# Optimization experiments

Measured on AMD Instinct MI355X. Metric: run time of the kernel, lower is better.

Reference implementation:

```python
import jax, jax.numpy as jnp
import numpy as np

N = 500000     # total nodes across all sets
DIM = 128      # input feature dim
HID = 128      # hidden_dim (output of key_net/val_net)
KDIM = 128     # key_storage.encoder.input_dim
MID = 128      # build_mlp mid width (midmult=1.0 -> (in+out)/2)
NB = 4096      # n_batches

def mish(x):
    return x * jnp.tanh(jax.nn.softplus(x))

def layernorm(x, g, b):
    mu = jnp.mean(x, axis=-1, keepdims=True)
    var = jnp.var(x, axis=-1, keepdims=True)
    return (x - mu) * jax.lax.rsqrt(var + 1e-5) * g + b

def mlp2(x, W1, b1, g, bn, W2, b2):
    # build_mlp(nlayers=2, layernorm=True, nonlinearity=Mish)
    h = layernorm(x @ W1 + b1, g, bn)
    return mish(h) @ W2 + b2

def seg_softmax(x, batch, n):
    # scatter_softmax over the node axis within each segment, per feature
    m = jax.ops.segment_max(x, batch, num_segments=n)
    e = jnp.exp(x - m[batch])
    d = jax.ops.segment_sum(e, batch, num_segments=n)
    return e / d[batch]

def _init(key, fan_in, shape):
    return jax.random.normal(key, shape, dtype=jnp.float32) / np.sqrt(fan_in)

def setup_inputs():
    key = jax.random.key(0)
    ks = jax.random.split(key, 12)
    return {
        "x": jax.random.normal(ks[0], (N, DIM), dtype=jnp.float32),
        "batch": jnp.sort(jax.random.randint(ks[1], (N,), 0, NB)),
        "n_batches": NB,
        # mapping: Linear(dim -> KDIM)
        "W_map": _init(ks[2], DIM, (DIM, KDIM)), "b_map": jnp.zeros(KDIM, jnp.float32),
        # key_net: KDIM -> MID -> HID
        "kW1": _init(ks[3], KDIM, (KDIM, MID)), "kb1": jnp.zeros(MID, jnp.float32),
        "kg": jnp.ones(MID, jnp.float32), "kbn": jnp.zeros(MID, jnp.float32),
        "kW2": _init(ks[4], MID, (MID, HID)), "kb2": jnp.zeros(HID, jnp.float32),
        # val_net: DIM -> MID -> HID
        "vW1": _init(ks[5], DIM, (DIM, MID)), "vb1": jnp.zeros(MID, jnp.float32),
        "vg": jnp.ones(MID, jnp.float32), "vbn": jnp.zeros(MID, jnp.float32),
        "vW2": _init(ks[6], MID, (MID, HID)), "vb2": jnp.zeros(HID, jnp.float32),
        # inner key_storage encoder params (same structure, on keys)
        "iW_map": _init(ks[7], KDIM, (KDIM, KDIM)), "ib_map": jnp.zeros(KDIM, jnp.float32),
        "ikW1": _init(ks[8], KDIM, (KDIM, MID)), "ikb1": jnp.zeros(MID, jnp.float32),
        "ikg": jnp.ones(MID, jnp.float32), "ikbn": jnp.zeros(MID, jnp.float32),
        "ikW2": _init(ks[9], MID, (MID, HID)), "ikb2": jnp.zeros(HID, jnp.float32),
        "ivW1": _init(ks[10], KDIM, (KDIM, MID)), "ivb1": jnp.zeros(MID, jnp.float32),
        "ivg": jnp.ones(MID, jnp.float32), "ivbn": jnp.zeros(MID, jnp.float32),
        "ivW2": _init(ks[11], MID, (MID, HID)), "ivb2": jnp.zeros(HID, jnp.float32),
    }

def reference(x, batch, n_batches, W_map, b_map, kW1, kb1, kg, kbn, kW2, kb2,
              vW1, vb1, vg, vbn, vW2, vb2, iW_map, ib_map,
              ikW1, ikb1, ikg, ikbn, ikW2, ikb2, ivW1, ivb1, ivg, ivbn, ivW2, ivb2):
    # key0 = mapping(x); keys = scatter_softmax(key0, batch)
    key0 = x @ W_map + b_map                      # [N, KDIM]
    keys = seg_softmax(key0, batch, n_batches)    # [N, KDIM]
    # y = val_net(x) * key_net(keys); z = scatter_sum(y, batch)
    y = mlp2(x, vW1, vb1, vg, vbn, vW2, vb2) * mlp2(keys, kW1, kb1, kg, kbn, kW2, kb2)
    z = jax.ops.segment_sum(y, batch, num_segments=n_batches)   # [NB, HID]
    # keyenc = key_storage.encoder(keys, batch): same encoder math applied to keys
    key0b = keys @ iW_map + ib_map
    keys2 = seg_softmax(key0b, batch, n_batches)
    y2 = mlp2(keys, ivW1, ivb1, ivg, ivbn, ivW2, ivb2) * mlp2(keys2, ikW1, ikb1, ikg, ikbn, ikW2, ikb2)
    keyenc = jax.ops.segment_sum(y2, batch, num_segments=n_batches)  # [NB, HID]
    return (z, keyenc)
```

## Files before the change

### kernel.cpp

```cpp
#include <hip/hip_runtime.h>

typedef _Float16 f16;
typedef _Float16 f16x4 __attribute__((ext_vector_type(4)));
typedef _Float16 f16x8 __attribute__((ext_vector_type(8)));
typedef float f32x4 __attribute__((ext_vector_type(4)));

#define NBATCH 4096
#define RMAX 200

__device__ __forceinline__ f32x4 mfma16(f16x8 a, f16x8 b, f32x4 c) {
  return __builtin_amdgcn_mfma_f32_16x16x32_f16(a, b, c, 0, 0, 0);
}

__device__ __forceinline__ int swz(int r, int c) { return r * 128 + (c ^ ((r & 7) << 3)); }

__global__ void seg_bounds(const int* __restrict__ batch, int N, int NB, int* __restrict__ seg) {
  int s = blockIdx.x * blockDim.x + threadIdx.x;
  if (s > NB) return;
  int lo = 0, hi = N;
  while (lo < hi) { int mid = (lo + hi) >> 1; if (batch[mid] < s) lo = mid + 1; else hi = mid; }
  seg[s] = lo;
}

__global__ void pack_weights(const float* w0, const float* w1, const float* w2, const float* w3,
                             const float* w4, const float* w5, const float* w6, const float* w7,
                             const float* w8, const float* w9, f16* __restrict__ Wp) {
  int idx = blockIdx.x * blockDim.x + threadIdx.x;
  if (idx >= 10 * 16384) return;
  int w = idx >> 14, p = idx & 16383;
  int j = p & 7, lane = (p >> 3) & 63, nt = (p >> 9) & 7, kk = p >> 12;
  int k = kk * 32 + (lane >> 4) * 8 + j;
  int n = nt * 16 + (lane & 15);
  const float* W;
  switch (w) {
    case 0: W = w0; break; case 1: W = w1; break; case 2: W = w2; break;
    case 3: W = w3; break; case 4: W = w4; break; case 5: W = w5; break;
    case 6: W = w6; break; case 7: W = w7; break; case 8: W = w8; break;
    default: W = w9; break;
  }
  Wp[idx] = (f16)W[k * 128 + n];
}

__device__ __forceinline__ void gemm_bias_phase(const f16* S, f16* D, const f16* __restrict__ Wg,
    const float* __restrict__ bias, int rows, int mh, int nq, int lane, int quad, int li) {
  int ntl = (rows + 15) >> 4;
  f16x8 bF[4][2];
#pragma unroll
  for (int kk = 0; kk < 4; ++kk)
#pragma unroll
    for (int j = 0; j < 2; ++j)
      bF[kk][j] = *(const f16x8*)(Wg + (size_t)(((kk * 8 + nq * 2 + j) * 64 + lane) * 8));
  float bc[2];
#pragma unroll
  for (int j = 0; j < 2; ++j) bc[j] = bias[(nq * 2 + j) * 16 + li];
  for (int t = mh; t < ntl; t += 2) {
    int m0 = t * 16;
    f32x4 acc0 = {0.f, 0.f, 0.f, 0.f}, acc1 = {0.f, 0.f, 0.f, 0.f};
    int rl = m0 + li;
    bool ok = rl < rows;
#pragma unroll
    for (int kk = 0; kk < 4; ++kk) {
      f16x8 aF = {};
      if (ok) aF = *(const f16x8*)(S + swz(rl, kk * 32 + quad * 8));
      acc0 = mfma16(aF, bF[kk][0], acc0);
      acc1 = mfma16(aF, bF[kk][1], acc1);
    }
#pragma unroll
    for (int r = 0; r < 4; ++r) {
      int row = m0 + quad * 4 + r;
      if (row < rows) {
        D[swz(row, (nq * 2) * 16 + li)] = (f16)(acc0[r] + bc[0]);
        D[swz(row, (nq * 2 + 1) * 16 + li)] = (f16)(acc1[r] + bc[1]);
      }
    }
  }
}

__device__ __forceinline__ void ln_mish_pass(f16* D, const float* __restrict__ g,
                                             const float* __restrict__ bn, int rows, int tid) {
  int part = tid & 3;
  float gv[32], bv[32];
#pragma unroll
  for (int j = 0; j < 8; ++j) {
    float4 gg = *(const float4*)(g + part * 32 + j * 4);
    float4 bb = *(const float4*)(bn + part * 32 + j * 4);
    gv[j * 4 + 0] = gg.x; gv[j * 4 + 1] = gg.y; gv[j * 4 + 2] = gg.z; gv[j * 4 + 3] = gg.w;
    bv[j * 4 + 0] = bb.x; bv[j * 4 + 1] = bb.y; bv[j * 4 + 2] = bb.z; bv[j * 4 + 3] = bb.w;
  }
  for (int r = tid >> 2; r < rows; r += 128) {
    f16x8 v[4];
    float s1 = 0.f, s2 = 0.f;
#pragma unroll
    for (int j = 0; j < 4; ++j) {
      v[j] = *(const f16x8*)(D + swz(r, part * 32 + j * 8));
#pragma unroll
      for (int e = 0; e < 8; ++e) { float f = (float)v[j][e]; s1 += f; s2 += f * f; }
    }
    s1 += __shfl_xor(s1, 1, 64); s2 += __shfl_xor(s2, 1, 64);
    s1 += __shfl_xor(s1, 2, 64); s2 += __shfl_xor(s2, 2, 64);
    float mean = s1 * (1.f / 128.f);
    float var = s2 * (1.f / 128.f) - mean * mean;
    float rstd = rsqrtf(var + 1e-5f);
#pragma unroll
    for (int j = 0; j < 4; ++j) {
      f16x8 o;
#pragma unroll
      for (int e = 0; e < 8; ++e) {
        float u = ((float)v[j][e] - mean) * rstd * gv[j * 8 + e] + bv[j * 8 + e];
        float t = __expf(u);
        float w = t * t + 2.f * t;
        float res = (u > 20.f) ? u : u * (w / (w + 2.f));
        o[e] = (f16)res;
      }
      *(f16x8*)(D + swz(r, part * 32 + j * 8)) = o;
    }
  }
}

__device__ __forceinline__ void softmax_phase(f16* P, int rows, int tid, float* sm, float* sd) {
  int c = tid & 127, st = tid >> 7;
  float m = -3.4e38f, d = 0.f;
#pragma unroll 4
  for (int r = st; r < rows; r += 4) {
    float v = (float)P[swz(r, c)];
    if (v > m) { d = d * __expf(m - v) + 1.f; m = v; } else d += __expf(v - m);
  }
  sm[st * 128 + c] = m; sd[st * 128 + c] = d;
  __syncthreads();
  if (tid < 128) {
    float M = sm[tid], D = sd[tid];
#pragma unroll
    for (int k = 1; k < 4; ++k) {
      float mk = sm[k * 128 + tid], dk = sd[k * 128 + tid];
      if (mk > M) { D = D * __expf(M - mk) + dk; M = mk; } else D += dk * __expf(mk - M);
    }
    sm[tid] = M; sd[tid] = (D > 0.f) ? 1.f / D : 0.f;
  }
  __syncthreads();
  float M = sm[c], inv = sd[c];
#pragma unroll 4
  for (int r = st; r < rows; r += 4)
    P[swz(r, c)] = (f16)(__expf((float)P[swz(r, c)] - M) * inv);
  __syncthreads();
}

__device__ __forceinline__ void pairsum_phase(const f16* S1, const f16* __restrict__ W1,
    const float* __restrict__ b1, const f16* S2, const f16* __restrict__ W2,
    const float* __restrict__ b2, float* __restrict__ outp, int s, int rows,
    int mh, int nq, int lane, int quad, int li, float* red, int tid) {
  f16x8 bF1[4][2], bF2[4][2];
#pragma unroll
  for (int kk = 0; kk < 4; ++kk)
#pragma unroll
    for (int j = 0; j < 2; ++j) {
      size_t off = (size_t)(((kk * 8 + nq * 2 + j) * 64 + lane) * 8);
      bF1[kk][j] = *(const f16x8*)(W1 + off);
      bF2[kk][j] = *(const f16x8*)(W2 + off);
    }
  float b1c[2], b2c[2];
#pragma unroll
  for (int j = 0; j < 2; ++j) {
    b1c[j] = b1[(nq * 2 + j) * 16 + li];
    b2c[j] = b2[(nq * 2 + j) * 16 + li];
  }
  float zs0 = 0.f, zs1 = 0.f;
  int ntl = (rows + 15) >> 4;
  for (int t = mh; t < ntl; t += 2) {
    int m0 = t * 16;
    f32x4 a10 = {0.f,0.f,0.f,0.f}, a11 = {0.f,0.f,0.f,0.f};
    f32x4 a20 = {0.f,0.f,0.f,0.f}, a21 = {0.f,0.f,0.f,0.f};
    int rl = m0 + li;
    bool ok = rl < rows;
#pragma unroll
    for (int kk = 0; kk < 4; ++kk) {
      f16x8 aF1 = {}, aF2 = {};
      if (ok) {
        aF1 = *(const f16x8*)(S1 + swz(rl, kk * 32 + quad * 8));
        aF2 = *(const f16x8*)(S2 + swz(rl, kk * 32 + quad * 8));
      }
      a10 = mfma16(aF1, bF1[kk][0], a10);
      a11 = mfma16(aF1, bF1[kk][1], a11);
      a20 = mfma16(aF2, bF2[kk][0], a20);
      a21 = mfma16(aF2, bF2[kk][1], a21);
    }
    float cs0 = 0.f, cs1 = 0.f;
#pragma unroll
    for (int r = 0; r < 4; ++r) {
      int row = m0 + quad * 4 + r;
      if (row < rows) {
        cs0 += (a10[r] + b1c[0]) * (a20[r] + b2c[0]);
        cs1 += (a11[r] + b1c[1]) * (a21[r] + b2c[1]);
      }
    }
    cs0 += __shfl_xor(cs0, 16, 64); cs0 += __shfl_xor(cs0, 32, 64);
    cs1 += __shfl_xor(cs1, 16, 64); cs1 += __shfl_xor(cs1, 32, 64);
    zs0 += cs0; zs1 += cs1;
  }
  red[tid] = 0.f; red[tid + 512] = 0.f;
  __syncthreads();
  if (quad == 0) {
    int w = tid >> 6;
    red[w * 128 + (nq * 2) * 16 + li] = zs0;
    red[w * 128 + (nq * 2 + 1) * 16 + li] = zs1;
  }
  __syncthreads();
  if (tid < 128) {
    float ssum = 0.f;
#pragma unroll
    for (int w = 0; w < 8; ++w) ssum += red[w * 128 + tid];
    outp[(size_t)s * 128 + tid] = ssum;
  }
  __syncthreads();
}

__global__ __launch_bounds__(512) void encoder_mega(
    const float* __restrict__ x, const int* __restrict__ seg, const f16* __restrict__ Wp,
    const float* b_map, const float* kb1, const float* kg, const float* kbn, const float* kb2,
    const float* vb1, const float* vg, const float* vbn, const float* vb2,
    const float* ib_map, const float* ikb1, const float* ikg, const float* ikbn,
    const float* ikb2, const float* ivb1, const float* ivg, const float* ivbn,
    const float* ivb2, float* __restrict__ Z, float* __restrict__ KE) {
  __shared__ f16 L0[RMAX * 128];
  __shared__ f16 L1[RMAX * 128];
  __shared__ f16 L2[RMAX * 128];
  __shared__ float red[8 * 128];
  __shared__ float sm[512];
  __shared__ float sd[512];
  int s = blockIdx.x;
  int a = seg[s], e = seg[s + 1];
  int rows = e - a;
  int tid = threadIdx.x;
  if (rows <= 0) {
    if (tid < 128) {
      Z[(size_t)s * 128 + tid] = 0.f;
      KE[(size_t)s * 128 + tid] = 0.f;
    }
    return;
  }
  if (rows > RMAX) rows = RMAX;
  int lane = tid & 63, wave = tid >> 6, quad = lane >> 4, li = lane & 15;
  int mh = wave & 1, nq = wave >> 1;

  const float* xa = x + (size_t)a * 128;
  for (int i = tid * 4; i < rows * 128; i += 2048) {
    float4 v = *(const float4*)(xa + i);
    f16x4 h;
    h[0] = (f16)v.x; h[1] = (f16)v.y; h[2] = (f16)v.z; h[3] = (f16)v.w;
    *(f16x4*)(L0 + swz(i >> 7, i & 127)) = h;
  }
  __syncthreads();
  gemm_bias_phase(L0, L1, Wp + 0 * 16384, b_map, rows, mh, nq, lane, quad, li);
  __syncthreads();
  softmax_phase(L1, rows, tid, sm, sd);
  gemm_bias_phase(L0, L2, Wp + 3 * 16384, vb1, rows, mh, nq, lane, quad, li);
  __syncthreads();
  ln_mish_pass(L2, vg, vbn, rows, tid);
  __syncthreads();
  gemm_bias_phase(L1, L0, Wp + 1 * 16384, kb1, rows, mh, nq, lane, quad, li);
  __syncthreads();
  ln_mish_pass(L0, kg, kbn, rows, tid);
  __syncthreads();
  pairsum_phase(L2, Wp + 4 * 16384, vb2, L0, Wp + 2 * 16384, kb2, Z, s, rows,
                mh, nq, lane, quad, li, red, tid);
  gemm_bias_phase(L1, L2, Wp + 5 * 16384, ib_map, rows, mh, nq, lane, quad, li);
  __syncthreads();
  softmax_phase(L2, rows, tid, sm, sd);
  gemm_bias_phase(L1, L0, Wp + 8 * 16384, ivb1, rows, mh, nq, lane, quad, li);
  __syncthreads();
  ln_mish_pass(L0, ivg, ivbn, rows, tid);
  __syncthreads();
  gemm_bias_phase(L2, L1, Wp + 6 * 16384, ikb1, rows, mh, nq, lane, quad, li);
  __syncthreads();
  ln_mish_pass(L1, ikg, ikbn, rows, tid);
  __syncthreads();
  pairsum_phase(L0, Wp + 9 * 16384, ivb2, L1, Wp + 7 * 16384, ikb2, KE, s, rows,
                mh, nq, lane, quad, li, red, tid);
}

extern "C" void kernel_launch(void* const* d_in, const int* in_sizes, int n_in,
                              void* d_out, int out_size, void* d_ws, size_t ws_size,
                              hipStream_t stream) {
  const float* x = (const float*)d_in[0];
  const int* batch = (const int*)d_in[1];
  const int N = in_sizes[1];
  const float* W_map = (const float*)d_in[3];  const float* b_map = (const float*)d_in[4];
  const float* kW1 = (const float*)d_in[5];    const float* kb1 = (const float*)d_in[6];
  const float* kg = (const float*)d_in[7];     const float* kbn = (const float*)d_in[8];
  const float* kW2 = (const float*)d_in[9];    const float* kb2 = (const float*)d_in[10];
  const float* vW1 = (const float*)d_in[11];   const float* vb1 = (const float*)d_in[12];
  const float* vg = (const float*)d_in[13];    const float* vbn = (const float*)d_in[14];
  const float* vW2 = (const float*)d_in[15];   const float* vb2 = (const float*)d_in[16];
  const float* iW_map = (const float*)d_in[17];const float* ib_map = (const float*)d_in[18];
  const float* ikW1 = (const float*)d_in[19];  const float* ikb1 = (const float*)d_in[20];
  const float* ikg = (const float*)d_in[21];   const float* ikbn = (const float*)d_in[22];
  const float* ikW2 = (const float*)d_in[23];  const float* ikb2 = (const float*)d_in[24];
  const float* ivW1 = (const float*)d_in[25];  const float* ivb1 = (const float*)d_in[26];
  const float* ivg = (const float*)d_in[27];   const float* ivbn = (const float*)d_in[28];
  const float* ivW2 = (const float*)d_in[29];  const float* ivb2 = (const float*)d_in[30];

  char* ws = (char*)d_ws;
  int* seg = (int*)ws;
  f16* Wp = (f16*)(ws + 32768);

  float* Z = (float*)d_out;
  float* KE = Z + (out_size / 2);

  seg_bounds<<<(NBATCH + 1 + 255) / 256, 256, 0, stream>>>(batch, N, NBATCH, seg);
  pack_weights<<<(10 * 16384) / 256, 256, 0, stream>>>(
      W_map, kW1, kW2, vW1, vW2, iW_map, ikW1, ikW2, ivW1, ivW2, Wp);

  encoder_mega<<<NBATCH, 512, 0, stream>>>(
      x, seg, Wp, b_map, kb1, kg, kbn, kb2, vb1, vg, vbn, vb2,
      ib_map, ikb1, ikg, ikbn, ikb2, ivb1, ivg, ivbn, ivb2, Z, KE);
}
```

Before: 1.287 ms.

## Double block size to 1024 threads and restructure segment softmax into register two-pass

Launches the fused encoder with 1024 threads per segment. Each wave now covers one of four row-tile phases, so every GEMM phase gets twice as many waves in flight. LayerNorm-Mish becomes single-row-per-thread, since 256 row slots cover RMAX, and weight-parameter loads move inside the row guard. Softmax now holds up to 25 values per thread in registers and computes max, then sum, then normalise, replacing the online max/sum. This avoids rereading LDS and the conditional exp rescaling, at the cost of more registers and extra barriers. Per-block register budget halves and the reduction scratch grows, which may reduce occupancy.

```diff
diff --git a/kernel.cpp b/kernel.cpp
--- a/kernel.cpp
+++ b/kernel.cpp
@@ -42,7 +42,7 @@
 }
 
 __device__ __forceinline__ void gemm_bias_phase(const f16* S, f16* D, const f16* __restrict__ Wg,
-    const float* __restrict__ bias, int rows, int mh, int nq, int lane, int quad, int li) {
+    const float* __restrict__ bias, int rows, int mq, int nq, int lane, int quad, int li) {
   int ntl = (rows + 15) >> 4;
   f16x8 bF[4][2];
 #pragma unroll
@@ -53,7 +53,7 @@
   float bc[2];
 #pragma unroll
   for (int j = 0; j < 2; ++j) bc[j] = bias[(nq * 2 + j) * 16 + li];
-  for (int t = mh; t < ntl; t += 2) {
+  for (int t = mq; t < ntl; t += 4) {
     int m0 = t * 16;
     f32x4 acc0 = {0.f, 0.f, 0.f, 0.f}, acc1 = {0.f, 0.f, 0.f, 0.f};
     int rl = m0 + li;
@@ -79,15 +79,16 @@
 __device__ __forceinline__ void ln_mish_pass(f16* D, const float* __restrict__ g,
                                              const float* __restrict__ bn, int rows, int tid) {
   int part = tid & 3;
-  float gv[32], bv[32];
-#pragma unroll
-  for (int j = 0; j < 8; ++j) {
-    float4 gg = *(const float4*)(g + part * 32 + j * 4);
-    float4 bb = *(const float4*)(bn + part * 32 + j * 4);
-    gv[j * 4 + 0] = gg.x; gv[j * 4 + 1] = gg.y; gv[j * 4 + 2] = gg.z; gv[j * 4 + 3] = gg.w;
-    bv[j * 4 + 0] = bb.x; bv[j * 4 + 1] = bb.y; bv[j * 4 + 2] = bb.z; bv[j * 4 + 3] = bb.w;
-  }
-  for (int r = tid >> 2; r < rows; r += 128) {
+  int r = tid >> 2;
+  if (r < rows) {
+    float gv[32], bv[32];
+#pragma unroll
+    for (int j = 0; j < 8; ++j) {
+      float4 gg = *(const float4*)(g + part * 32 + j * 4);
+      float4 bb = *(const float4*)(bn + part * 32 + j * 4);
+      gv[j * 4 + 0] = gg.x; gv[j * 4 + 1] = gg.y; gv[j * 4 + 2] = gg.z; gv[j * 4 + 3] = gg.w;
+      bv[j * 4 + 0] = bb.x; bv[j * 4 + 1] = bb.y; bv[j * 4 + 2] = bb.z; bv[j * 4 + 3] = bb.w;
+    }
     f16x8 v[4];
     float s1 = 0.f, s2 = 0.f;
 #pragma unroll
@@ -117,37 +118,53 @@
   }
 }
 
-__device__ __forceinline__ void softmax_phase(f16* P, int rows, int tid, float* sm, float* sd) {
+__device__ __forceinline__ void softmax_phase(f16* P, int rows, int tid, float* scr) {
   int c = tid & 127, st = tid >> 7;
-  float m = -3.4e38f, d = 0.f;
-#pragma unroll 4
-  for (int r = st; r < rows; r += 4) {
-    float v = (float)P[swz(r, c)];
-    if (v > m) { d = d * __expf(m - v) + 1.f; m = v; } else d += __expf(v - m);
-  }
-  sm[st * 128 + c] = m; sd[st * 128 + c] = d;
+  float v[25];
+#pragma unroll
+  for (int i = 0; i < 25; ++i) {
+    int r = st + i * 8;
+    v[i] = (r < rows) ? (float)P[swz(r, c)] : -3.4e38f;
+  }
+  float m = v[0];
+#pragma unroll
+  for (int i = 1; i < 25; ++i) m = fmaxf(m, v[i]);
+  scr[st * 128 + c] = m;
   __syncthreads();
   if (tid < 128) {
-    float M = sm[tid], D = sd[tid];
-#pragma unroll
-    for (int k = 1; k < 4; ++k) {
-      float mk = sm[k * 128 + tid], dk = sd[k * 128 + tid];
-      if (mk > M) { D = D * __expf(M - mk) + dk; M = mk; } else D += dk * __expf(mk - M);
-    }
-    sm[tid] = M; sd[tid] = (D > 0.f) ? 1.f / D : 0.f;
-  }
-  __syncthreads();
-  float M = sm[c], inv = sd[c];
-#pragma unroll 4
-  for (int r = st; r < rows; r += 4)
-    P[swz(r, c)] = (f16)(__expf((float)P[swz(r, c)] - M) * inv);
+    float M = scr[tid];
+#pragma unroll
+    for (int k = 1; k < 8; ++k) M = fmaxf(M, scr[k * 128 + tid]);
+    scr[tid] = M;
+  }
+  __syncthreads();
+  float M = scr[c];
+  float d = 0.f;
+#pragma unroll
+  for (int i = 0; i < 25; ++i) { v[i] = __expf(v[i] - M); d += v[i]; }
+  __syncthreads();
+  scr[st * 128 + c] = d;
+  __syncthreads();
+  if (tid < 128) {
+    float D = 0.f;
+#pragma unroll
+    for (int k = 0; k < 8; ++k) D += scr[k * 128 + tid];
+    scr[tid] = (D > 0.f) ? 1.f / D : 0.f;
+  }
+  __syncthreads();
+  float inv = scr[c];
+#pragma unroll
+  for (int i = 0; i < 25; ++i) {
+    int r = st + i * 8;
+    if (r < rows) P[swz(r, c)] = (f16)(v[i] * inv);
+  }
   __syncthreads();
 }
 
 __device__ __forceinline__ void pairsum_phase(const f16* S1, const f16* __restrict__ W1,
     const float* __restrict__ b1, const f16* S2, const f16* __restrict__ W2,
     const float* __restrict__ b2, float* __restrict__ outp, int s, int rows,
-    int mh, int nq, int lane, int quad, int li, float* red, int tid) {
+    int mq, int nq, int lane, int quad, int li, float* red, int tid) {
   f16x8 bF1[4][2], bF2[4][2];
 #pragma unroll
   for (int kk = 0; kk < 4; ++kk)
@@ -165,7 +182,7 @@
   }
   float zs0 = 0.f, zs1 = 0.f;
   int ntl = (rows + 15) >> 4;
-  for (int t = mh; t < ntl; t += 2) {
+  for (int t = mq; t < ntl; t += 4) {
     int m0 = t * 16;
     f32x4 a10 = {0.f,0.f,0.f,0.f}, a11 = {0.f,0.f,0.f,0.f};
     f32x4 a20 = {0.f,0.f,0.f,0.f}, a21 = {0.f,0.f,0.f,0.f};
@@ -196,24 +213,24 @@
     cs1 += __shfl_xor(cs1, 16, 64); cs1 += __shfl_xor(cs1, 32, 64);
     zs0 += cs0; zs1 += cs1;
   }
-  red[tid] = 0.f; red[tid + 512] = 0.f;
+  int wave = tid >> 6;
+  red[tid] = 0.f; red[tid + 1024] = 0.f;
   __syncthreads();
   if (quad == 0) {
-    int w = tid >> 6;
-    red[w * 128 + (nq * 2) * 16 + li] = zs0;
-    red[w * 128 + (nq * 2 + 1) * 16 + li] = zs1;
+    red[wave * 128 + (nq * 2) * 16 + li] = zs0;
+    red[wave * 128 + (nq * 2 + 1) * 16 + li] = zs1;
   }
   __syncthreads();
   if (tid < 128) {
     float ssum = 0.f;
 #pragma unroll
-    for (int w = 0; w < 8; ++w) ssum += red[w * 128 + tid];
+    for (int w = 0; w < 16; ++w) ssum += red[w * 128 + tid];
     outp[(size_t)s * 128 + tid] = ssum;
   }
   __syncthreads();
 }
 
-__global__ __launch_bounds__(512) void encoder_mega(
+__global__ __launch_bounds__(1024) void encoder_mega(
     const float* __restrict__ x, const int* __restrict__ seg, const f16* __restrict__ Wp,
     const float* b_map, const float* kb1, const float* kg, const float* kbn, const float* kb2,
     const float* vb1, const float* vg, const float* vbn, const float* vb2,
@@ -223,9 +240,7 @@
   __shared__ f16 L0[RMAX * 128];
   __shared__ f16 L1[RMAX * 128];
   __shared__ f16 L2[RMAX * 128];
-  __shared__ float red[8 * 128];
-  __shared__ float sm[512];
-  __shared__ float sd[512];
+  __shared__ float scr[2048];
   int s = blockIdx.x;
   int a = seg[s], e = seg[s + 1];
   int rows = e - a;
@@ -239,42 +254,42 @@
   }
   if (rows > RMAX) rows = RMAX;
   int lane = tid & 63, wave = tid >> 6, quad = lane >> 4, li = lane & 15;
-  int mh = wave & 1, nq = wave >> 1;
+  int mq = wave & 3, nq = wave >> 2;
 
   const float* xa = x + (size_t)a * 128;
-  for (int i = tid * 4; i < rows * 128; i += 2048) {
+  for (int i = tid * 4; i < rows * 128; i += 4096) {
     float4 v = *(const float4*)(xa + i);
     f16x4 h;
     h[0] = (f16)v.x; h[1] = (f16)v.y; h[2] = (f16)v.z; h[3] = (f16)v.w;
     *(f16x4*)(L0 + swz(i >> 7, i & 127)) = h;
   }
   __syncthreads();
-  gemm_bias_phase(L0, L1, Wp + 0 * 16384, b_map, rows, mh, nq, lane, quad, li);
-  __syncthreads();
-  softmax_phase(L1, rows, tid, sm, sd);
-  gemm_bias_phase(L0, L2, Wp + 3 * 16384, vb1, rows, mh, nq, lane, quad, li);
+  gemm_bias_phase(L0, L1, Wp + 0 * 16384, b_map, rows, mq, nq, lane, quad, li);
+  __syncthreads();
+  softmax_phase(L1, rows, tid, scr);
+  gemm_bias_phase(L0, L2, Wp + 3 * 16384, vb1, rows, mq, nq, lane, quad, li);
   __syncthreads();
   ln_mish_pass(L2, vg, vbn, rows, tid);
   __syncthreads();
-  gemm_bias_phase(L1, L0, Wp + 1 * 16384, kb1, rows, mh, nq, lane, quad, li);
+  gemm_bias_phase(L1, L0, Wp + 1 * 16384, kb1, rows, mq, nq, lane, quad, li);
   __syncthreads();
   ln_mish_pass(L0, kg, kbn, rows, tid);
   __syncthreads();
   pairsum_phase(L2, Wp + 4 * 16384, vb2, L0, Wp + 2 * 16384, kb2, Z, s, rows,
-                mh, nq, lane, quad, li, red, tid);
-  gemm_bias_phase(L1, L2, Wp + 5 * 16384, ib_map, rows, mh, nq, lane, quad, li);
-  __syncthreads();
-  softmax_phase(L2, rows, tid, sm, sd);
-  gemm_bias_phase(L1, L0, Wp + 8 * 16384, ivb1, rows, mh, nq, lane, quad, li);
+                mq, nq, lane, quad, li, scr, tid);
+  gemm_bias_phase(L1, L2, Wp + 5 * 16384, ib_map, rows, mq, nq, lane, quad, li);
+  __syncthreads();
+  softmax_phase(L2, rows, tid, scr);
+  gemm_bias_phase(L1, L0, Wp + 8 * 16384, ivb1, rows, mq, nq, lane, quad, li);
   __syncthreads();
   ln_mish_pass(L0, ivg, ivbn, rows, tid);
   __syncthreads();
-  gemm_bias_phase(L2, L1, Wp + 6 * 16384, ikb1, rows, mh, nq, lane, quad, li);
+  gemm_bias_phase(L2, L1, Wp + 6 * 16384, ikb1, rows, mq, nq, lane, quad, li);
   __syncthreads();
   ln_mish_pass(L1, ikg, ikbn, rows, tid);
   __syncthreads();
   pairsum_phase(L0, Wp + 9 * 16384, ivb2, L1, Wp + 7 * 16384, ikb2, KE, s, rows,
-                mh, nq, lane, quad, li, red, tid);
+                mq, nq, lane, quad, li, scr, tid);
 }
 
 extern "C" void kernel_launch(void* const* d_in, const int* in_sizes, int n_in,
@@ -309,7 +324,7 @@
   pack_weights<<<(10 * 16384) / 256, 256, 0, stream>>>(
       W_map, kW1, kW2, vW1, vW2, iW_map, ikW1, ikW2, ivW1, ivW2, Wp);
 
-  encoder_mega<<<NBATCH, 512, 0, stream>>>(
+  encoder_mega<<<NBATCH, 1024, 0, stream>>>(
       x, seg, Wp, b_map, kb1, kg, kbn, kb2, vb1, vg, vbn, vb2,
       ib_map, ikb1, ikg, ikbn, ikb2, ivb1, ivg, ivbn, ivb2, Z, KE);
 }
```

New measurement: 1.473 ms. 14.4% more time.
